# Kernel tuning notes

Measured on AMD Instinct MI355X. Metric: run time of the kernel, lower is better.

The kernel has to match this reference:

```python
import jax, jax.numpy as jnp
import numpy as np

B, S, HID = 2, 2048, 2048
H, D = 16, 128
BASE = 10000.0
NEG = -1e9


def _rope_tables(seq_len, dim, dtype):
    inv_freq = 1.0 / (BASE ** (jnp.arange(0, dim, 2, dtype=jnp.float32) / dim))
    pos = jnp.arange(seq_len, dtype=jnp.float32)
    freqs = jnp.einsum('s,d->sd', pos, inv_freq)          # [S, D/2]
    emb = jnp.concatenate([freqs, freqs], axis=-1)        # [S, D]
    return jnp.cos(emb).astype(dtype), jnp.sin(emb).astype(dtype)


def _rotate_half(x):
    x1, x2 = jnp.split(x, 2, axis=-1)
    return jnp.concatenate([-x2, x1], axis=-1)


def setup_inputs() -> dict:
    key = jax.random.key(0)
    k1, k2, k3 = jax.random.split(key, 3)
    x = jax.random.normal(k1, (B, S, HID), dtype=jnp.float32)
    w_qkv = jax.random.normal(k2, (HID, 3 * HID), dtype=jnp.float32) * (HID ** -0.5)
    w_out = jax.random.normal(k3, (HID, HID), dtype=jnp.float32) * (HID ** -0.5)
    return {"x": x, "w_qkv": w_qkv, "w_out": w_out}


def reference(x, w_qkv, w_out):
    b, s, _ = x.shape
    qkv = x @ w_qkv                                        # [B, S, 3*HID]
    qkv = qkv.reshape(b, s, 3, H, D).transpose(2, 0, 3, 1, 4)  # [3, B, H, S, D]
    q, k, v = qkv[0], qkv[1], qkv[2]
    cos, sin = _rope_tables(s, D, x.dtype)                 # [S, D]
    cos = cos[None, None]
    sin = sin[None, None]
    q = q * cos + _rotate_half(q) * sin
    k = k * cos + _rotate_half(k) * sin
    scale = 1.0 / np.sqrt(D)
    scores = jnp.einsum('bhqd,bhkd->bhqk', q, k) * scale   # [B, H, S, S]
    causal = jnp.triu(jnp.ones((s, s), dtype=bool), k=1)
    scores = jnp.where(causal[None, None], NEG, scores)
    attn = jax.nn.softmax(scores, axis=-1)
    out = jnp.einsum('bhqk,bhkd->bhqd', attn, v)           # [B, H, S, D]
    out = out.transpose(0, 2, 1, 3).reshape(b, s, H * D)
    return out @ w_out
```

## Files before the change

### kernel.cpp

```cpp
#include <hip/hip_runtime.h>
#include <hip/hip_bf16.h>

#define S_LEN 2048
#define HID_DIM 2048
#define NH 16
#define HD 128
#define N3 6144

typedef __bf16 bf16x8 __attribute__((ext_vector_type(8)));
typedef unsigned short u16x8 __attribute__((ext_vector_type(8)));
typedef float f32x4 __attribute__((ext_vector_type(4)));
typedef float f32x16 __attribute__((ext_vector_type(16)));

#define MFMA16(a, b, c) __builtin_amdgcn_mfma_f32_16x16x32_bf16(a, b, c, 0, 0, 0)
#define MFMA32(a, b, c) __builtin_amdgcn_mfma_f32_32x32x16_bf16(a, b, c, 0, 0, 0)

__device__ __forceinline__ unsigned short f2bf(float f) {
  union { float f; unsigned u; } v; v.f = f;
  return (unsigned short)((v.u + 0x7fffu + ((v.u >> 16) & 1u)) >> 16);
}
__device__ __forceinline__ float bf2f(unsigned short h) {
  union { unsigned u; float f; } v; v.u = ((unsigned)h) << 16; return v.f;
}
__device__ __forceinline__ unsigned packbf2(float lo, float hi) {
  union { __hip_bfloat162 h2; unsigned u; } cv;
  cv.h2 = __float22bfloat162_rn(make_float2(lo, hi));
  return cv.u;
}
__device__ __forceinline__ void store_c(float* p, float v) { *p = v; }
__device__ __forceinline__ void store_c(unsigned short* p, float v) { *p = f2bf(v); }

__device__ __forceinline__ void async16(const void* g, void* l) {
  __builtin_amdgcn_global_load_lds((const __attribute__((address_space(1))) unsigned int*)g,
                                   (__attribute__((address_space(3))) unsigned int*)l,
                                   16, 0, 0);
}

template <int N> __device__ __forceinline__ void vmcnt();
template <> __device__ __forceinline__ void vmcnt<0>() { asm volatile("s_waitcnt vmcnt(0)" ::: "memory"); }
template <> __device__ __forceinline__ void vmcnt<5>() { asm volatile("s_waitcnt vmcnt(5)" ::: "memory"); }
template <> __device__ __forceinline__ void vmcnt<6>() { asm volatile("s_waitcnt vmcnt(6)" ::: "memory"); }

#define PLSWAP(a, b) asm volatile("v_permlane32_swap_b32 %0, %1" : "+v"(a), "+v"(b))

__global__ __launch_bounds__(256) void cast_bf16(const float4* __restrict__ src,
                                                 ushort4* __restrict__ dst) {
  int i = blockIdx.x * 256 + threadIdx.x;
  float4 v = src[i];
  ushort4 o;
  o.x = f2bf(v.x); o.y = f2bf(v.y); o.z = f2bf(v.z); o.w = f2bf(v.w);
  dst[i] = o;
}

__global__ __launch_bounds__(256) void transpose_cast(const float* __restrict__ src,
                                                      unsigned short* __restrict__ dst,
                                                      int R, int Ccols) {
  __shared__ float t[32][33];
  int ct = Ccols >> 5;
  int bx = blockIdx.x % ct, by = blockIdx.x / ct;
  int c0 = bx << 5, r0 = by << 5;
  int lx = threadIdx.x & 31, ly = threadIdx.x >> 5;
#pragma unroll
  for (int i = 0; i < 32; i += 8)
    t[ly + i][lx] = src[(long long)(r0 + ly + i) * Ccols + c0 + lx];
  __syncthreads();
#pragma unroll
  for (int i = 0; i < 32; i += 8)
    dst[(long long)(c0 + ly + i) * R + r0 + lx] = f2bf(t[lx][ly + i]);
}

__global__ __launch_bounds__(256) void rope_tables(float* __restrict__ cosT,
                                                   float* __restrict__ sinT) {
  int idx = blockIdx.x * 256 + threadIdx.x;
  int s = idx >> 6, i = idx & 63;
  float invf = powf(10000.0f, -(float)i * (1.0f / 64.0f));
  float a = (float)s * invf;
  cosT[idx] = cosf(a);
  sinT[idx] = sinf(a);
}

__global__ __launch_bounds__(512) void gemm256(const unsigned short* __restrict__ A,
                                               const unsigned short* __restrict__ Bt,
                                               unsigned short* __restrict__ C,
                                               int Mdim, int Ncols, int ldc, int Kdim) {
  constexpr int AEL = 256 * 64, BUFE = 2 * AEL;
  __shared__ unsigned short smem[2 * BUFE];

  const int ntn = Ncols >> 8;
  const int nwg = (Mdim >> 8) * ntn;
  int bid = blockIdx.x;
  bid = (bid & 7) * (nwg >> 3) + (bid >> 3);
  const int tm = (bid / ntn) << 8;
  const int tn = (bid % ntn) << 8;

  const int tid = threadIdx.x;
  const int w = tid >> 6, l = tid & 63;
  const int g = l >> 4, cc = l & 15;
  const int wm = w >> 2, wn = w & 3;

  const int srow = tid >> 3;
  const int schunk = (tid & 7) ^ (srow & 7);
  const unsigned short* gA = A + (long long)(tm + srow) * Kdim + schunk * 8;
  const unsigned short* gB = Bt + (long long)(tn + srow) * Kdim + schunk * 8;

  const int ch0 = ((g) ^ (cc & 7)) << 3;
  const int ch1 = ((4 + g) ^ (cc & 7)) << 3;

  f32x4 acc[8][4] = {};
  bf16x8 a[4][2], b[4][2];
  const int nk = Kdim >> 6;

#define ST_A(kt2, BUF, s) \
  async16(gA + (long long)(s) * 64 * Kdim + ((long long)(kt2) << 6), \
          smem + (BUF) * BUFE + (s) * 4096 + w * 512)
#define ST_B(kt2, BUF, s) \
  async16(gB + (long long)(s) * 64 * Kdim + ((long long)(kt2) << 6), \
          smem + (BUF) * BUFE + AEL + (s) * 4096 + w * 512)

#pragma unroll
  for (int s = 0; s < 4; ++s) ST_A(0, 0, s);
#pragma unroll
  for (int s = 0; s < 4; ++s) ST_B(0, 0, s);
  ST_A(1, 1, 0); ST_A(1, 1, 2);
  ST_B(1, 1, 0); ST_B(1, 1, 1); ST_B(1, 1, 2); ST_B(1, 1, 3);
  vmcnt<6>();
  __builtin_amdgcn_s_barrier();

#define KSTEP(kt, BUF, OBUF)                                                      \
  {                                                                               \
    const unsigned short* Ab = smem + (BUF) * BUFE + wm * (128 * 64);             \
    const unsigned short* Bb = smem + (BUF) * BUFE + AEL + wn * (64 * 64);        \
                    \
    _Pragma("unroll") for (int i = 0; i < 4; ++i) {                               \
      const int r = (i * 16 + cc) << 6;                                           \
      a[i][0] = *(const bf16x8*)(Ab + r + ch0);                                   \
      a[i][1] = *(const bf16x8*)(Ab + r + ch1);                                   \
    }                                                                             \
    _Pragma("unroll") for (int j = 0; j < 2; ++j) {                               \
      const int r = (j * 16 + cc) << 6;                                           \
      b[j][0] = *(const bf16x8*)(Bb + r + ch0);                                   \
      b[j][1] = *(const bf16x8*)(Bb + r + ch1);                                   \
    }                                                                             \
    if ((kt) + 1 < nk) { ST_A((kt) + 1, OBUF, 1); ST_A((kt) + 1, OBUF, 3); }      \
    __builtin_amdgcn_s_barrier();                                                 \
    __builtin_amdgcn_s_setprio(1);                                                \
    _Pragma("unroll") for (int i = 0; i < 4; ++i)                                 \
      _Pragma("unroll") for (int j = 0; j < 2; ++j) {                             \
        acc[i][j] = MFMA16(a[i][0], b[j][0], acc[i][j]);                          \
        acc[i][j] = MFMA16(a[i][1], b[j][1], acc[i][j]);                          \
      }                                                                           \
    __builtin_amdgcn_s_setprio(0);                                                \
    __builtin_amdgcn_s_barrier();                                                 \
                                              \
    _Pragma("unroll") for (int j = 0; j < 2; ++j) {                               \
      const int r = ((2 + j) * 16 + cc) << 6;                                     \
      b[2 + j][0] = *(const bf16x8*)(Bb + r + ch0);                               \
      b[2 + j][1] = *(const bf16x8*)(Bb + r + ch1);                               \
    }                                                                             \
    if ((kt) + 2 < nk) { ST_A((kt) + 2, BUF, 0); ST_A((kt) + 2, BUF, 2); }        \
    __builtin_amdgcn_s_barrier();                                                 \
    __builtin_amdgcn_s_setprio(1);                                                \
    _Pragma("unroll") for (int i = 0; i < 4; ++i)                                 \
      _Pragma("unroll") for (int j = 0; j < 2; ++j) {                             \
        acc[i][2 + j] = MFMA16(a[i][0], b[2 + j][0], acc[i][2 + j]);              \
        acc[i][2 + j] = MFMA16(a[i][1], b[2 + j][1], acc[i][2 + j]);              \
      }                                                                           \
    __builtin_amdgcn_s_setprio(0);                                                \
    __builtin_amdgcn_s_barrier();                                                 \
                                              \
    _Pragma("unroll") for (int i = 0; i < 4; ++i) {                               \
      const int r = ((64 + i * 16 + cc) << 6);                                    \
      a[i][0] = *(const bf16x8*)(Ab + r + ch0);                                   \
      a[i][1] = *(const bf16x8*)(Ab + r + ch1);                                   \
    }                                                                             \
    if ((kt) + 2 < nk) { ST_B((kt) + 2, BUF, 0); ST_B((kt) + 2, BUF, 1); }        \
    __builtin_amdgcn_s_barrier();                                                 \
    __builtin_amdgcn_s_setprio(1);                                                \
    _Pragma("unroll") for (int i = 0; i < 4; ++i)                                 \
      _Pragma("unroll") for (int j = 0; j < 2; ++j) {                             \
        acc[4 + i][j] = MFMA16(a[i][0], b[j][0], acc[4 + i][j]);                  \
        acc[4 + i][j] = MFMA16(a[i][1], b[j][1], acc[4 + i][j]);                  \
      }                                                                           \
    __builtin_amdgcn_s_setprio(0);                                                \
    __builtin_amdgcn_s_barrier();                                                 \
                            \
    if ((kt) + 2 < nk) { ST_B((kt) + 2, BUF, 2); ST_B((kt) + 2, BUF, 3); }        \
    __builtin_amdgcn_s_barrier();                                                 \
    __builtin_amdgcn_s_setprio(1);                                                \
    _Pragma("unroll") for (int i = 0; i < 4; ++i)                                 \
      _Pragma("unroll") for (int j = 0; j < 2; ++j) {                             \
        acc[4 + i][2 + j] = MFMA16(a[i][0], b[2 + j][0], acc[4 + i][2 + j]);      \
        acc[4 + i][2 + j] = MFMA16(a[i][1], b[2 + j][1], acc[4 + i][2 + j]);      \
      }                                                                           \
    __builtin_amdgcn_s_setprio(0);                                                \
    if ((kt) + 2 < nk) vmcnt<6>(); else vmcnt<0>();                               \
    __builtin_amdgcn_s_barrier();                                                 \
  }

  for (int kt = 0; kt < nk; kt += 2) {
    KSTEP(kt, 0, 1);
    KSTEP(kt + 1, 1, 0);
  }
#undef KSTEP
#undef ST_A
#undef ST_B

  const int crow0 = tm + wm * 128;
  const int ccol0 = tn + wn * 64;
#pragma unroll
  for (int i = 0; i < 8; ++i)
#pragma unroll
    for (int j = 0; j < 4; ++j)
#pragma unroll
      for (int p = 0; p < 4; ++p) {
        int row = crow0 + i * 16 + (g << 2) + p;
        int col = ccol0 + j * 16 + cc;
        store_c(&C[(long long)row * ldc + col], acc[i][j][p]);
      }
}

template <int BM, int BN, typename OutT>
__global__ __launch_bounds__(512) void gemm_pipe8(const unsigned short* __restrict__ A,
                                                  const unsigned short* __restrict__ Bt,
                                                  OutT* __restrict__ C,
                                                  int Mdim, int Ncols, int ldc, int Kdim) {
  constexpr int WTM = BM / 2, WTN = BN / 4;
  constexpr int MREP = WTM / 16, NREP = WTN / 16;
  constexpr int AEL = BM * 64, BEL = BN * 64, BUFE = AEL + BEL;
  constexpr int AINST = BM / 64, BINST = BN / 64;
  constexpr int AHALF = BM / 128, BHALF = BN / 128;
  constexpr int VN = BN / 64 + BM / 128;
  __shared__ unsigned short smem[2 * BUFE];

  const int ntn = Ncols / BN;
  const int nwg = (Mdim / BM) * ntn;
  int bid = blockIdx.x;
  bid = (bid & 7) * (nwg >> 3) + (bid >> 3);
  const int tm = (bid / ntn) * BM;
  const int tn = (bid % ntn) * BN;

  const int tid = threadIdx.x;
  const int w = tid >> 6, l = tid & 63;
  const int g = l >> 4, cc = l & 15;
  const int wm = w >> 2, wn = w & 3;

  const int srow = tid >> 3;
  const int schunk = (tid & 7) ^ (srow & 7);
  const unsigned short* gA = A + (long long)(tm + srow) * Kdim + schunk * 8;
  const unsigned short* gB = Bt + (long long)(tn + srow) * Kdim + schunk * 8;

  const int ch0 = ((g) ^ (cc & 7)) << 3;
  const int ch1 = ((4 + g) ^ (cc & 7)) << 3;

  f32x4 acc[MREP][NREP] = {};
  bf16x8 a[MREP / 2][2], b[NREP][2];

  const int nk = Kdim >> 6;

#define STAGE_A(kt2, s) \
  async16(gA + (long long)(s) * 64 * Kdim + ((long long)(kt2) << 6), \
          smem + ((kt2) & 1) * BUFE + (s) * 4096 + w * 512)
#define STAGE_B(kt2, s) \
  async16(gB + (long long)(s) * 64 * Kdim + ((long long)(kt2) << 6), \
          smem + ((kt2) & 1) * BUFE + AEL + (s) * 4096 + w * 512)

#pragma unroll
  for (int s = 0; s < AINST; ++s) STAGE_A(0, s);
#pragma unroll
  for (int s = 0; s < BINST; ++s) STAGE_B(0, s);
#pragma unroll
  for (int s = 0; s < BINST; ++s) STAGE_B(1, s);
#pragma unroll
  for (int s = 0; s < AHALF; ++s) STAGE_A(1, s);
  vmcnt<VN>();
  __builtin_amdgcn_s_barrier();

  for (int kt = 0; kt < nk; ++kt) {
    const int buf = kt & 1;
    const unsigned short* Ab = smem + buf * BUFE + (wm * WTM) * 64;
    const unsigned short* Bb = smem + buf * BUFE + AEL + (wn * WTN) * 64;

#pragma unroll
    for (int i = 0; i < MREP / 2; ++i) {
      const int r = (i * 16 + cc) << 6;
      a[i][0] = *(const bf16x8*)(Ab + r + ch0);
      a[i][1] = *(const bf16x8*)(Ab + r + ch1);
    }
#pragma unroll
    for (int j = 0; j < NREP; ++j) {
      const int r = (j * 16 + cc) << 6;
      b[j][0] = *(const bf16x8*)(Bb + r + ch0);
      b[j][1] = *(const bf16x8*)(Bb + r + ch1);
    }
    if (kt + 1 < nk) {
#pragma unroll
      for (int s = AHALF; s < AINST; ++s) STAGE_A(kt + 1, s);
    }
    __builtin_amdgcn_s_barrier();
    __builtin_amdgcn_s_setprio(1);
#pragma unroll
    for (int i = 0; i < MREP / 2; ++i)
#pragma unroll
      for (int j = 0; j < NREP / 2; ++j) {
        acc[i][j] = MFMA16(a[i][0], b[j][0], acc[i][j]);
        acc[i][j] = MFMA16(a[i][1], b[j][1], acc[i][j]);
      }
    __builtin_amdgcn_s_setprio(0);
    __builtin_amdgcn_s_barrier();

    if (kt + 2 < nk) {
#pragma unroll
      for (int s = 0; s < BHALF; ++s) STAGE_B(kt + 2, s);
    }
    __builtin_amdgcn_s_barrier();
    __builtin_amdgcn_s_setprio(1);
#pragma unroll
    for (int i = 0; i < MREP / 2; ++i)
#pragma unroll
      for (int j = 0; j < NREP / 2; ++j) {
        f32x4& ac = acc[i][NREP / 2 + j];
        ac = MFMA16(a[i][0], b[NREP / 2 + j][0], ac);
        ac = MFMA16(a[i][1], b[NREP / 2 + j][1], ac);
      }
    __builtin_amdgcn_s_setprio(0);
    __builtin_amdgcn_s_barrier();

#pragma unroll
    for (int i = 0; i < MREP / 2; ++i) {
      const int r = ((WTM / 2) + i * 16 + cc) << 6;
      a[i][0] = *(const bf16x8*)(Ab + r + ch0);
      a[i][1] = *(const bf16x8*)(Ab + r + ch1);
    }
    if (kt + 2 < nk) {
#pragma unroll
      for (int s = BHALF; s < BINST; ++s) STAGE_B(kt + 2, s);
    }
    __builtin_amdgcn_s_barrier();
    __builtin_amdgcn_s_setprio(1);
#pragma unroll
    for (int i = 0; i < MREP / 2; ++i)
#pragma unroll
      for (int j = 0; j < NREP / 2; ++j) {
        f32x4& ac = acc[MREP / 2 + i][j];
        ac = MFMA16(a[i][0], b[j][0], ac);
        ac = MFMA16(a[i][1], b[j][1], ac);
      }
    __builtin_amdgcn_s_setprio(0);
    __builtin_amdgcn_s_barrier();

    if (kt + 2 < nk) {
#pragma unroll
      for (int s = 0; s < AHALF; ++s) STAGE_A(kt + 2, s);
    }
    __builtin_amdgcn_s_barrier();
    __builtin_amdgcn_s_setprio(1);
#pragma unroll
    for (int i = 0; i < MREP / 2; ++i)
#pragma unroll
      for (int j = 0; j < NREP / 2; ++j) {
        f32x4& ac = acc[MREP / 2 + i][NREP / 2 + j];
        ac = MFMA16(a[i][0], b[NREP / 2 + j][0], ac);
        ac = MFMA16(a[i][1], b[NREP / 2 + j][1], ac);
      }
    __builtin_amdgcn_s_setprio(0);
    if (kt + 2 < nk) vmcnt<VN>(); else vmcnt<0>();
    __builtin_amdgcn_s_barrier();
  }
#undef STAGE_A
#undef STAGE_B

  const int crow0 = tm + wm * WTM;
  const int ccol0 = tn + wn * WTN;
#pragma unroll
  for (int i = 0; i < MREP; ++i)
#pragma unroll
    for (int j = 0; j < NREP; ++j)
#pragma unroll
      for (int p = 0; p < 4; ++p) {
        int row = crow0 + i * 16 + (g << 2) + p;
        int col = ccol0 + j * 16 + cc;
        store_c(&C[(long long)row * ldc + col], acc[i][j][p]);
      }
}

__global__ __launch_bounds__(256) void split_rope(const unsigned short* __restrict__ qkv,
                                                  const float* __restrict__ cosT,
                                                  const float* __restrict__ sinT,
                                                  unsigned short* __restrict__ Qb,
                                                  unsigned short* __restrict__ Kb,
                                                  unsigned short* __restrict__ Vt) {
  __shared__ unsigned short vtile[32][128];
  const int bid = blockIdx.x;
  const int st = bid & 63;
  const int h = (bid >> 6) & 15;
  const int b = bid >> 10;
  const int s0 = st << 5;
  const int t = threadIdx.x;
  const float qscale = 0.08838834764831845f;

  {
    const int sl = t >> 3;
    const int d0 = (t & 7) << 3;
    const int s = s0 + sl;
    const long long rb = ((long long)(b * S_LEN + s)) * N3 + h * HD;
    u16x8 qlo = *(const u16x8*)(qkv + rb + d0);
    u16x8 qhi = *(const u16x8*)(qkv + rb + 64 + d0);
    u16x8 klo = *(const u16x8*)(qkv + rb + HID_DIM + d0);
    u16x8 khi = *(const u16x8*)(qkv + rb + HID_DIM + 64 + d0);
    const float* cp = cosT + (s << 6) + d0;
    const float* sp = sinT + (s << 6) + d0;
    f32x4 c0 = *(const f32x4*)(cp), c1 = *(const f32x4*)(cp + 4);
    f32x4 sn0 = *(const f32x4*)(sp), sn1 = *(const f32x4*)(sp + 4);
    u16x8 qo_lo, qo_hi, ko_lo, ko_hi;
#pragma unroll
    for (int j = 0; j < 8; ++j) {
      float cv = (j < 4) ? c0[j & 3] : c1[j & 3];
      float sv = (j < 4) ? sn0[j & 3] : sn1[j & 3];
      float ql = bf2f(qlo[j]), qh = bf2f(qhi[j]);
      float kl = bf2f(klo[j]), kh = bf2f(khi[j]);
      qo_lo[j] = f2bf((ql * cv - qh * sv) * qscale);
      qo_hi[j] = f2bf((qh * cv + ql * sv) * qscale);
      ko_lo[j] = f2bf(kl * cv - kh * sv);
      ko_hi[j] = f2bf(kh * cv + kl * sv);
    }
    const long long ob = ((long long)((b * NH + h) * S_LEN + s)) * HD + d0;
    *(u16x8*)(Qb + ob) = qo_lo;
    *(u16x8*)(Qb + ob + 64) = qo_hi;
    *(u16x8*)(Kb + ob) = ko_lo;
    *(u16x8*)(Kb + ob + 64) = ko_hi;
  }

  {
    const int sl = t >> 3;
    const int d0 = (t & 7) << 4;
    const int s = s0 + sl;
    const long long vb_in = ((long long)(b * S_LEN + s)) * N3 + h * HD + 2 * HID_DIM;
    u16x8 v0 = *(const u16x8*)(qkv + vb_in + d0);
    u16x8 v1 = *(const u16x8*)(qkv + vb_in + d0 + 8);
    *(u16x8*)(&vtile[sl][d0]) = v0;
    *(u16x8*)(&vtile[sl][d0 + 8]) = v1;
  }
  __syncthreads();
  {
    const int dr = t >> 1;
    const int sh = (t & 1) << 4;
    unsigned short tv[16];
#pragma unroll
    for (int j = 0; j < 16; ++j) tv[j] = vtile[sh + j][dr];
    uint4 u0, u1;
    u0.x = (unsigned)tv[0] | ((unsigned)tv[1] << 16);
    u0.y = (unsigned)tv[2] | ((unsigned)tv[3] << 16);
    u0.z = (unsigned)tv[4] | ((unsigned)tv[5] << 16);
    u0.w = (unsigned)tv[6] | ((unsigned)tv[7] << 16);
    u1.x = (unsigned)tv[8] | ((unsigned)tv[9] << 16);
    u1.y = (unsigned)tv[10] | ((unsigned)tv[11] << 16);
    u1.z = (unsigned)tv[12] | ((unsigned)tv[13] << 16);
    u1.w = (unsigned)tv[14] | ((unsigned)tv[15] << 16);
    const long long vb = ((long long)((b * NH + h) * HD + dr)) * S_LEN + s0 + sh;
    *(uint4*)(Vt + vb) = u0;
    *(uint4*)(Vt + vb + 8) = u1;
  }
}

__global__ __launch_bounds__(256) void flash_attn(const unsigned short* __restrict__ Qg,
                                                  const unsigned short* __restrict__ Kg,
                                                  const unsigned short* __restrict__ Vt,
                                                  unsigned short* __restrict__ Ob) {
  __shared__ unsigned short smem[32768];
  const int id = blockIdx.x;
  const int bh = id & 31;
  const int qtr = (id >> 5) & 7;
  const int qt = (id >> 8) ? qtr : 15 - qtr;
  const int Q0 = qt << 7;
  const int b = bh >> 4, h = bh & 15;
  const long long base = (long long)bh * (S_LEN * HD);
  const int tid = threadIdx.x, w = tid >> 6, l = tid & 63;
  const int hi = l >> 5, q = l & 31;
  const int q0w = Q0 + (w << 5);
  const int g = l >> 4, c = l & 15;

  bf16x8 qf[8];
  {
    const unsigned short* qp = Qg + base + (long long)(q0w + q) * HD + (hi << 3);
#pragma unroll
    for (int s = 0; s < 8; ++s) qf[s] = *(const bf16x8*)(qp + (s << 4));
  }

  f32x16 oacc[4] = {};
  float m = -1e30f, lsum = 0.f;

  const int nt = (qt << 1) + 2;

  auto STAGE = [&](int kv0, int buf) {
    unsigned short* ks = smem + buf * 8192;
    unsigned short* vs = smem + 16384 + buf * 8192;
#pragma unroll
    for (int j = 0; j < 4; ++j) {
      int row = (w << 4) + (j << 2) + g;
      int chunk = c ^ (row & 7);
      async16(Kg + base + (long long)(kv0 + row) * HD + (chunk << 3),
              ks + (((w << 4) + (j << 2)) << 7));
    }
#pragma unroll
    for (int j = 0; j < 4; ++j) {
      int dr = (w << 5) + (j << 3) + (l >> 3);
      int chunk = (l & 7) ^ (dr & 7);
      async16(Vt + base + (long long)dr * S_LEN + kv0 + (chunk << 3),
              vs + (((w << 5) + (j << 3)) << 6));
    }
  };

  STAGE(0, 0);
  __syncthreads();

  int cur = 0;
  for (int t = 0; t < nt; ++t) {
    const int kv0 = t << 6;
    if (t + 1 < nt) STAGE((t + 1) << 6, cur ^ 1);

    if (kv0 < q0w + 32) {
      const unsigned short* ks = smem + cur * 8192;
      const unsigned short* vs = smem + 16384 + cur * 8192;

      f32x16 sa[2] = {};
#pragma unroll
      for (int h2 = 0; h2 < 2; ++h2) {
        const char* kb = (const char*)ks + (((h2 << 5) + q) << 8);
        const int r7 = q & 7;
#pragma unroll
        for (int s = 0; s < 8; ++s) {
          bf16x8 kf = *(const bf16x8*)(kb + ((((s << 1) + hi) ^ r7) << 4));
          sa[h2] = MFMA32(kf, qf[s], sa[h2]);
        }
      }

      if (kv0 + 63 > q0w) {
        const int qq = q0w + q;
#pragma unroll
        for (int h2 = 0; h2 < 2; ++h2)
#pragma unroll
          for (int j = 0; j < 16; ++j) {
            int kv = kv0 + (h2 << 5) + (j & 3) + ((j >> 2) << 3) + (hi << 2);
            if (kv > qq) sa[h2][j] = -1e30f;
          }
      }

      float t0 = sa[0][0], t1 = sa[0][1], t2 = sa[0][2], t3 = sa[0][3];
#pragma unroll
      for (int j = 4; j < 16; j += 4) {
        t0 = fmaxf(t0, sa[0][j]);     t1 = fmaxf(t1, sa[0][j + 1]);
        t2 = fmaxf(t2, sa[0][j + 2]); t3 = fmaxf(t3, sa[0][j + 3]);
      }
#pragma unroll
      for (int j = 0; j < 16; j += 4) {
        t0 = fmaxf(t0, sa[1][j]);     t1 = fmaxf(t1, sa[1][j + 1]);
        t2 = fmaxf(t2, sa[1][j + 2]); t3 = fmaxf(t3, sa[1][j + 3]);
      }
      float tmax = fmaxf(fmaxf(t0, t1), fmaxf(t2, t3));
      {
        float tcp;
        asm volatile("v_mov_b32 %0, %1" : "=v"(tcp) : "v"(tmax));
        PLSWAP(tmax, tcp);
        tmax = fmaxf(tmax, tcp);
      }
      float mn = fmaxf(m, tmax);
      float fsc = __expf(m - mn);
      m = mn;
      float s0 = 0.f, s1 = 0.f, s2 = 0.f, s3 = 0.f;
#pragma unroll
      for (int h2 = 0; h2 < 2; ++h2)
#pragma unroll
        for (int j = 0; j < 16; j += 4) {
          float p0 = __expf(sa[h2][j] - mn);
          float p1 = __expf(sa[h2][j + 1] - mn);
          float p2 = __expf(sa[h2][j + 2] - mn);
          float p3 = __expf(sa[h2][j + 3] - mn);
          sa[h2][j] = p0; sa[h2][j + 1] = p1;
          sa[h2][j + 2] = p2; sa[h2][j + 3] = p3;
          s0 += p0; s1 += p1; s2 += p2; s3 += p3;
        }
      float ps = (s0 + s1) + (s2 + s3);
      {
        float pcp;
        asm volatile("v_mov_b32 %0, %1" : "=v"(pcp) : "v"(ps));
        PLSWAP(ps, pcp);
        ps = ps + pcp;
      }
      lsum = lsum * fsc + ps;
#pragma unroll
      for (int db = 0; db < 4; ++db)
#pragma unroll
        for (int j = 0; j < 16; ++j) oacc[db][j] *= fsc;

      unsigned up[2][8];
#pragma unroll
      for (int h2 = 0; h2 < 2; ++h2)
#pragma unroll
        for (int k = 0; k < 8; ++k)
          up[h2][k] = packbf2(sa[h2][2 * k], sa[h2][2 * k + 1]);
      union Frag { unsigned u[4]; bf16x8 v; } pf[4];
#pragma unroll
      for (int s = 0; s < 4; ++s) {
        int h2 = s >> 1, q4 = (s & 1) << 2;
        unsigned a0 = up[h2][q4 + 0], b0 = up[h2][q4 + 2];
        unsigned a1 = up[h2][q4 + 1], b1 = up[h2][q4 + 3];
        PLSWAP(a0, b0);
        PLSWAP(a1, b1);
        pf[s].u[0] = a0; pf[s].u[1] = a1;
        pf[s].u[2] = b0; pf[s].u[3] = b1;
      }

#pragma unroll
      for (int db = 0; db < 4; ++db) {
        const char* vb = (const char*)vs + (((db << 5) + q) << 7);
        const int d7 = q & 7;
#pragma unroll
        for (int s = 0; s < 4; ++s) {
          bf16x8 vf = *(const bf16x8*)(vb + ((((s << 1) + hi) ^ d7) << 4));
          oacc[db] = MFMA32(vf, pf[s].v, oacc[db]);
        }
      }
    }

    __syncthreads();
    cur ^= 1;
  }

  const float rl = 1.0f / lsum;
#pragma unroll
  for (int db = 0; db < 4; ++db)
#pragma unroll
    for (int jg = 0; jg < 4; ++jg) {
      int d = (db << 5) + (jg << 3) + (hi << 2);
      unsigned v0 = packbf2(oacc[db][4 * jg] * rl, oacc[db][4 * jg + 1] * rl);
      unsigned v1 = packbf2(oacc[db][4 * jg + 2] * rl, oacc[db][4 * jg + 3] * rl);
      *(uint2*)(smem + (((w << 5) + q) << 7) + d) = make_uint2(v0, v1);
    }
  __syncthreads();
  {
    const int qr = tid >> 1;
    const int dh = (tid & 1) << 6;
    const uint4* src = (const uint4*)(smem + (qr << 7) + dh);
    uint4* dst = (uint4*)(Ob + (long long)((b << 11) + Q0 + qr) * HID_DIM + (h << 7) + dh);
#pragma unroll
    for (int cc2 = 0; cc2 < 8; ++cc2) dst[cc2] = src[cc2];
  }
}

extern "C" void kernel_launch(void* const* d_in, const int* in_sizes, int n_in,
                              void* d_out, int out_size, void* d_ws, size_t ws_size,
                              hipStream_t stream) {
  (void)in_sizes; (void)n_in; (void)out_size; (void)ws_size;
  const float* x = (const float*)d_in[0];
  const float* w_qkv = (const float*)d_in[1];
  const float* w_out = (const float*)d_in[2];
  float* out = (float*)d_out;
  char* ws = (char*)d_ws;

  unsigned short* xb    = (unsigned short*)(ws);
  unsigned short* wqkvT = (unsigned short*)(ws + 16777216);
  unsigned short* woutT = (unsigned short*)(ws + 41943040);
  unsigned short* qkv   = (unsigned short*)(ws + 50331648);
  unsigned short* Qb    = (unsigned short*)(ws + 100663296);
  unsigned short* Kb    = (unsigned short*)(ws + 117440512);
  unsigned short* Vt    = (unsigned short*)(ws + 134217728);
  float* cosT = (float*)(ws + 150994944);
  float* sinT = (float*)(ws + 151519232);
  unsigned short* Ob = qkv;

  cast_bf16<<<8192, 256, 0, stream>>>((const float4*)x, (ushort4*)xb);
  transpose_cast<<<12288, 256, 0, stream>>>(w_qkv, wqkvT, 2048, 6144);
  transpose_cast<<<4096, 256, 0, stream>>>(w_out, woutT, 2048, 2048);
  rope_tables<<<512, 256, 0, stream>>>(cosT, sinT);
  gemm256<<<256, 512, 0, stream>>>(xb, wqkvT, qkv, 4096, 4096, 6144, 2048);
  gemm_pipe8<128, 256, unsigned short><<<256, 512, 0, stream>>>(
      xb, wqkvT + (long long)4096 * 2048, qkv + 4096, 4096, 2048, 6144, 2048);
  split_rope<<<2048, 256, 0, stream>>>(qkv, cosT, sinT, Qb, Kb, Vt);
  flash_attn<<<512, 256, 0, stream>>>(Qb, Kb, Vt, Ob);
  gemm_pipe8<128, 256, float><<<256, 512, 0, stream>>>(Ob, woutT, out, 4096, 2048, 2048, 2048);
}
```

Before: 271.6 us.

## Fuse prep kernels, add lazy softmax rescaling and MFMA priority hints

Merges the four preprocessing kernels (x cast, two weight transpose-casts, rope tables) into one launch to cut launch overhead and tail gaps. In flash attention, the running max and the output/sum rescale are only updated when some lane's tile max exceeds the current max by more than a threshold (ln 256), which skips the per-tile 64-element accumulator rescale. It also raises wave priority around the MFMA blocks. Lazy rescaling lets exponentials grow up to 256x before renormalizing, which carries some numerical-range risk, and the shared LDS array is now allocated for every block of the fused kernel.

```diff
diff --git a/kernel.cpp b/kernel.cpp
--- a/kernel.cpp
+++ b/kernel.cpp
@@ -43,35 +43,46 @@
 
 #define PLSWAP(a, b) asm volatile("v_permlane32_swap_b32 %0, %1" : "+v"(a), "+v"(b))
 
-__global__ __launch_bounds__(256) void cast_bf16(const float4* __restrict__ src,
-                                                 ushort4* __restrict__ dst) {
-  int i = blockIdx.x * 256 + threadIdx.x;
-  float4 v = src[i];
-  ushort4 o;
-  o.x = f2bf(v.x); o.y = f2bf(v.y); o.z = f2bf(v.z); o.w = f2bf(v.w);
-  dst[i] = o;
-}
-
-__global__ __launch_bounds__(256) void transpose_cast(const float* __restrict__ src,
-                                                      unsigned short* __restrict__ dst,
-                                                      int R, int Ccols) {
+__global__ __launch_bounds__(256) void prep_all(const float4* __restrict__ x4,
+                                                ushort4* __restrict__ xb4,
+                                                const float* __restrict__ w_qkv,
+                                                unsigned short* __restrict__ wqkvT,
+                                                const float* __restrict__ w_out,
+                                                unsigned short* __restrict__ woutT,
+                                                float* __restrict__ cosT,
+                                                float* __restrict__ sinT) {
   __shared__ float t[32][33];
-  int ct = Ccols >> 5;
-  int bx = blockIdx.x % ct, by = blockIdx.x / ct;
-  int c0 = bx << 5, r0 = by << 5;
-  int lx = threadIdx.x & 31, ly = threadIdx.x >> 5;
-#pragma unroll
-  for (int i = 0; i < 32; i += 8)
-    t[ly + i][lx] = src[(long long)(r0 + ly + i) * Ccols + c0 + lx];
-  __syncthreads();
-#pragma unroll
-  for (int i = 0; i < 32; i += 8)
-    dst[(long long)(c0 + ly + i) * R + r0 + lx] = f2bf(t[lx][ly + i]);
-}
-
-__global__ __launch_bounds__(256) void rope_tables(float* __restrict__ cosT,
-                                                   float* __restrict__ sinT) {
-  int idx = blockIdx.x * 256 + threadIdx.x;
+  int bid = blockIdx.x;
+  const int tid = threadIdx.x;
+
+  if (bid < 8192) {
+    int i = bid * 256 + tid;
+    float4 v = x4[i];
+    ushort4 o;
+    o.x = f2bf(v.x); o.y = f2bf(v.y); o.z = f2bf(v.z); o.w = f2bf(v.w);
+    xb4[i] = o;
+    return;
+  }
+  bid -= 8192;
+  if (bid < 12288 + 4096) {
+    const float* src; unsigned short* dst; int R, Ccols;
+    if (bid < 12288) { src = w_qkv; dst = wqkvT; R = 2048; Ccols = 6144; }
+    else { bid -= 12288; src = w_out; dst = woutT; R = 2048; Ccols = 2048; }
+    int ct = Ccols >> 5;
+    int bx = bid % ct, by = bid / ct;
+    int c0 = bx << 5, r0 = by << 5;
+    int lx = tid & 31, ly = tid >> 5;
+#pragma unroll
+    for (int i = 0; i < 32; i += 8)
+      t[ly + i][lx] = src[(long long)(r0 + ly + i) * Ccols + c0 + lx];
+    __syncthreads();
+#pragma unroll
+    for (int i = 0; i < 32; i += 8)
+      dst[(long long)(c0 + ly + i) * R + r0 + lx] = f2bf(t[lx][ly + i]);
+    return;
+  }
+  bid -= 16384;
+  int idx = bid * 256 + tid;
   int s = idx >> 6, i = idx & 63;
   float invf = powf(10000.0f, -(float)i * (1.0f / 64.0f));
   float a = (float)s * invf;
@@ -523,6 +534,7 @@
       const unsigned short* vs = smem + 16384 + cur * 8192;
 
       f32x16 sa[2] = {};
+      __builtin_amdgcn_s_setprio(1);
 #pragma unroll
       for (int h2 = 0; h2 < 2; ++h2) {
         const char* kb = (const char*)ks + (((h2 << 5) + q) << 8);
@@ -533,6 +545,7 @@
           sa[h2] = MFMA32(kf, qf[s], sa[h2]);
         }
       }
+      __builtin_amdgcn_s_setprio(0);
 
       if (kv0 + 63 > q0w) {
         const int qq = q0w + q;
@@ -563,18 +576,25 @@
         PLSWAP(tmax, tcp);
         tmax = fmaxf(tmax, tcp);
       }
-      float mn = fmaxf(m, tmax);
-      float fsc = __expf(m - mn);
-      m = mn;
+      if (__any(tmax > m + 5.545177444479562f)) {
+        float mn = fmaxf(m, tmax);
+        float fsc = __expf(m - mn);
+        m = mn;
+        lsum *= fsc;
+#pragma unroll
+        for (int db = 0; db < 4; ++db)
+#pragma unroll
+          for (int j = 0; j < 16; ++j) oacc[db][j] *= fsc;
+      }
       float s0 = 0.f, s1 = 0.f, s2 = 0.f, s3 = 0.f;
 #pragma unroll
       for (int h2 = 0; h2 < 2; ++h2)
 #pragma unroll
         for (int j = 0; j < 16; j += 4) {
-          float p0 = __expf(sa[h2][j] - mn);
-          float p1 = __expf(sa[h2][j + 1] - mn);
-          float p2 = __expf(sa[h2][j + 2] - mn);
-          float p3 = __expf(sa[h2][j + 3] - mn);
+          float p0 = __expf(sa[h2][j] - m);
+          float p1 = __expf(sa[h2][j + 1] - m);
+          float p2 = __expf(sa[h2][j + 2] - m);
+          float p3 = __expf(sa[h2][j + 3] - m);
           sa[h2][j] = p0; sa[h2][j + 1] = p1;
           sa[h2][j + 2] = p2; sa[h2][j + 3] = p3;
           s0 += p0; s1 += p1; s2 += p2; s3 += p3;
@@ -586,11 +606,7 @@
         PLSWAP(ps, pcp);
         ps = ps + pcp;
       }
-      lsum = lsum * fsc + ps;
-#pragma unroll
-      for (int db = 0; db < 4; ++db)
-#pragma unroll
-        for (int j = 0; j < 16; ++j) oacc[db][j] *= fsc;
+      lsum += ps;
 
       unsigned up[2][8];
 #pragma unroll
@@ -610,6 +626,7 @@
         pf[s].u[2] = b0; pf[s].u[3] = b1;
       }
 
+      __builtin_amdgcn_s_setprio(1);
 #pragma unroll
       for (int db = 0; db < 4; ++db) {
         const char* vb = (const char*)vs + (((db << 5) + q) << 7);
@@ -620,6 +637,7 @@
           oacc[db] = MFMA32(vf, pf[s].v, oacc[db]);
         }
       }
+      __builtin_amdgcn_s_setprio(0);
     }
 
     __syncthreads();
@@ -668,10 +686,8 @@
   float* sinT = (float*)(ws + 151519232);
   unsigned short* Ob = qkv;
 
-  cast_bf16<<<8192, 256, 0, stream>>>((const float4*)x, (ushort4*)xb);
-  transpose_cast<<<12288, 256, 0, stream>>>(w_qkv, wqkvT, 2048, 6144);
-  transpose_cast<<<4096, 256, 0, stream>>>(w_out, woutT, 2048, 2048);
-  rope_tables<<<512, 256, 0, stream>>>(cosT, sinT);
+  prep_all<<<25088, 256, 0, stream>>>((const float4*)x, (ushort4*)xb,
+                                      w_qkv, wqkvT, w_out, woutT, cosT, sinT);
   gemm256<<<256, 512, 0, stream>>>(xb, wqkvT, qkv, 4096, 4096, 6144, 2048);
   gemm_pipe8<128, 256, unsigned short><<<256, 512, 0, stream>>>(
       xb, wqkvT + (long long)4096 * 2048, qkv + 4096, 4096, 2048, 6144, 2048);
```

After: 288.5 us. 1.06x slower.
